# Optimization experiments

Hardware: AMD Instinct MI355X
Metric: run time of the kernel (lower is better)

The kernel has to match this reference:

```python
import jax, jax.numpy as jnp
import numpy as np

SEQ, B, T = 512, 1024, 48

def setup_inputs() -> dict:
    key = jax.random.key(0)
    k1, k2, k3, k4, k5 = jax.random.split(key, 5)
    return {
        "emissions": jax.random.normal(k1, (SEQ, B, T), dtype=jnp.float32),
        "tags": jax.random.randint(k2, (SEQ, B), 0, T, dtype=jnp.int64),
        "mask": jnp.ones((SEQ, B), dtype=jnp.int32),
        "start_transitions": jax.random.uniform(k3, (T,), minval=-0.1, maxval=0.1, dtype=jnp.float32),
        "end_transitions": jax.random.uniform(k4, (T,), minval=-0.1, maxval=0.1, dtype=jnp.float32),
        "transitions": jax.random.uniform(k5, (T, T), minval=-0.1, maxval=0.1, dtype=jnp.float32),
    }

def _score(emissions, tags, maskf, start_transitions, end_transitions, transitions):
    # numerator: score of the given tag path
    seq_len, batch = tags.shape
    emit = jnp.take_along_axis(emissions, tags[:, :, None], axis=2)[:, :, 0]  # (S,B)
    trans = transitions[tags[:-1], tags[1:]]  # (S-1,B)
    score = start_transitions[tags[0]] + emit[0]
    score = score + jnp.sum((trans + emit[1:]) * maskf[1:], axis=0)
    seq_ends = maskf.astype(jnp.int32).sum(axis=0) - 1  # (B,)
    last_tags = tags[seq_ends, jnp.arange(batch)]
    return score + end_transitions[last_tags]

def _normalizer(emissions, maskb, start_transitions, end_transitions, transitions):
    # forward algorithm: sequential logsumexp recurrence
    init = start_transitions + emissions[0]  # (B,T)

    def step(score, inp):
        emis_i, mask_i = inp  # (B,T), (B,)
        # score[b, prev] + transitions[prev, next] + emis_i[b, next]
        nxt = jax.nn.logsumexp(score[:, :, None] + transitions[None, :, :] + emis_i[:, None, :], axis=1)
        score = jnp.where(mask_i[:, None], nxt, score)
        return score, None

    score, _ = jax.lax.scan(step, init, (emissions[1:], maskb[1:]))
    return jax.nn.logsumexp(score + end_transitions, axis=1)

def reference(emissions, tags, mask, start_transitions, end_transitions, transitions):
    maskf = mask.astype(emissions.dtype)
    maskb = mask.astype(bool)
    num = _score(emissions, tags, maskf, start_transitions, end_transitions, transitions)
    den = _normalizer(emissions, maskb, start_transitions, end_transitions, transitions)
    llh = num - den  # (B,)
    return llh.mean()  # reduction='mean'
```

## Files before the change

### kernel.cpp

```cpp
#include <hip/hip_runtime.h>


constexpr int SEQ = 512, BN = 1024, TT = 48;
constexpr int CH = 8;
#define LOG2E 1.44269504088896340736f
#define LN2   0.69314718055994530942f

typedef int i32x4 __attribute__((ext_vector_type(4)));
typedef _Float16 h16x2 __attribute__((ext_vector_type(2)));

__device__ __forceinline__ float fexp2(float x) { return __builtin_amdgcn_exp2f(x); }
__device__ __forceinline__ float flog2(float x) { return __builtin_amdgcn_logf(x); }
__device__ __forceinline__ float rlane(float v, int i) {
    return __int_as_float(__builtin_amdgcn_readlane(__float_as_int(v), i));
}
__device__ __forceinline__ float dppswap(float v) {
    return __int_as_float(__builtin_amdgcn_mov_dpp(__float_as_int(v), 0xB1, 0xF, 0xF, true));
}
__device__ __forceinline__ float fdot2(int a, int b, float c) {
#if __has_builtin(__builtin_amdgcn_fdot2)
    return __builtin_amdgcn_fdot2(__builtin_bit_cast(h16x2, a),
                                  __builtin_bit_cast(h16x2, b), c, false);
#else
    float r;
    asm("v_dot2_f32_f16 %0, %1, %2, %3" : "=v"(r) : "v"(a), "v"(b), "v"(c));
    return r;
#endif
}

__global__ __launch_bounds__(128, 4) void crf_fwd(
    const float* __restrict__ emis, const int* __restrict__ tags,
    const int* __restrict__ mask, const float* __restrict__ start_t,
    const float* __restrict__ end_t, const float* __restrict__ trans,
    float* __restrict__ ws)
{
    __shared__ __align__(16) float smem[1600];

    const int tid  = threadIdx.x;
    const int wid  = tid >> 6;
    const int lane = tid & 63;
    const int cid  = blockIdx.x * 2 + wid;
    const int b    = cid & 1023;
    const int seg  = cid >> 10;
    const int cstart = seg ? (16 * seg - 1) : 0;
    const int cend   = 16 * (seg + 1);
    const int wbase  = wid * 768;
    int* pb = (int*)(smem + 1536) + wid * 32;

    const bool jv = (lane < TT);
    const int jc = jv ? lane : (TT - 1);
    const int l7 = lane & 7;

    _Float16* lh = (_Float16*)smem;
    for (int i = tid; i < TT * TT; i += 128) lh[i] = (_Float16)trans[i];
    __syncthreads();
    int Epk[24];
#pragma unroll
    for (int k = 0; k < 24; ++k) {
        const float a  = fexp2((float)lh[(2 * k) * TT + jc] * LOG2E);
        const float bb = fexp2((float)lh[(2 * k + 1) * TT + jc] * LOG2E);
        _Float16 h0 = (_Float16)a, h1 = (_Float16)bb;
        Epk[k] = (int)((unsigned)__builtin_bit_cast(unsigned short, h0) |
                       ((unsigned)__builtin_bit_cast(unsigned short, h1) << 16));
    }
#pragma unroll
    for (int k = 0; k < 24; ++k)
        asm volatile("" : "+v"(Epk[k]));
    const float st = start_t[jc];
    const float en = end_t[jc];
    __syncthreads();

    int offs[2];
#pragma unroll
    for (int k = 0; k < 2; ++k) {
        const int g = k * 64 + lane;
        const int r = g / 12, j4 = g % 12;
        offs[k] = r * (BN * TT * 4) + j4 * 16;
    }

#define STAGE_CHUNK(cc, buf)                                                   \
    {                                                                          \
        const char* cb = (const char*)emis + ((size_t)(cc) * CH * BN + b) * (TT * 4); \
        __builtin_amdgcn_global_load_lds(                                      \
            (const __attribute__((address_space(1))) void*)(cb + offs[0]),     \
            (__attribute__((address_space(3))) void*)(&smem[wbase + (buf) * 384]), \
            16, 0, 0);                                                         \
        if (lane < 32)                                                         \
            __builtin_amdgcn_global_load_lds(                                  \
                (const __attribute__((address_space(1))) void*)(cb + offs[1]), \
                (__attribute__((address_space(3))) void*)(&smem[wbase + (buf) * 384 + 256]), \
                16, 0, 0);                                                     \
    }

    STAGE_CHUNK(cstart, 0);
    int tgv = tags[(size_t)(cstart * CH + l7) * BN + b];
    int mkv = mask[(size_t)(cstart * CH + l7) * BN + b];

    asm volatile("s_waitcnt vmcnt(0)" ::: "memory");
    __builtin_amdgcn_sched_barrier(0);

    float r, numpart;
    int la, carry_tag;
    if (seg == 0) {
        const int tag0 = tags[b];
        const float e00 = smem[wbase + jc];
        r = jv ? fexp2(fmaf(st + e00, LOG2E, -6.0f)) : 0.0f;
        la = 6;
        numpart = (lane == tag0) ? (st + e00) : 0.f;
        carry_tag = tag0;
    } else {
        r = jv ? 1.0f : 0.0f;
        la = 0;
        numpart = 0.f;
        carry_tag = 0;
    }
    float numtr = 0.f, numem = 0.f, W = 0.f;
    int mcount = 0;

    STAGE_CHUNK(cstart + 1, 1);
    int tgn = tags[(size_t)((cstart + 1) * CH + l7) * BN + b];
    int mkn = mask[(size_t)((cstart + 1) * CH + l7) * BN + b];

    int cur = 0;

#pragma unroll 1
    for (int c = cstart; c < cend; ++c) {
#pragma unroll
        for (int k = 0; k < 24; ++k)
            asm volatile("" : "+v"(Epk[k]));

        const int tbase = c * CH;
        const float* ebc = smem + wbase + cur * 384;
        const bool warm = (c < 16 * seg);

        const int tmv = (lane < 8 && mkv && (tbase + lane) > 0) ? tgv : -1;
        const unsigned long long vmword = __ballot(tmv >= 0);
        int tprev = __shfl_up(tgv, 1, 64);
        if (lane == 0) tprev = carry_tag;
        if (!warm) {
            if (tmv >= 0) {
                numtr += trans[tprev * TT + tgv];
                numem += ebc[lane * TT + tgv];
            }
            mcount += __popcll(__ballot(lane < 8 && mkv));
        }
        carry_tag = __builtin_amdgcn_readlane(tgv, 7);
        la += 6 * (int)__popcll(vmword);

        const unsigned gm = (unsigned)vmword & 0xFFu;
        {
            const float r0 = rlane(r, 0);
            const int m = ((__float_as_int(r0) >> 23) & 0xFF) - 127;
            const float scl = __int_as_float((127 - m) << 23);
            r *= scl;
            la += m;
        }

        float emul[8];
#pragma unroll
        for (int u = 0; u < 8; ++u)
            emul[u] = fexp2(fmaf(ebc[u * TT + jc], LOG2E, -6.0f));

#pragma unroll
        for (int u = 0; u < 8; ++u) {
            const float rx = dppswap(r);
            const int pkw = __builtin_bit_cast(int,
                __builtin_amdgcn_cvt_pkrtz(r, rx));
            if (jv && !(lane & 1)) pb[lane >> 1] = pkw;
            asm volatile("" ::: "memory");
            const i32x4* pv = (const i32x4*)pb;
            float q0 = 0.f, q1 = 0.f, q2 = 0.f, q3 = 0.f;
#pragma unroll
            for (int k = 0; k < 6; ++k) {
                const i32x4 w = pv[k];
                q0 = fdot2(w.x, Epk[4 * k],     q0);
                q1 = fdot2(w.y, Epk[4 * k + 1], q1);
                q2 = fdot2(w.z, Epk[4 * k + 2], q2);
                q3 = fdot2(w.w, Epk[4 * k + 3], q3);
            }
            const float q = (q0 + q1) + (q2 + q3);
            const bool commit = (gm >> u) & 1u;
            r = commit ? (q * emul[u]) : r;
        }

        asm volatile("s_waitcnt vmcnt(0)" ::: "memory");
        __builtin_amdgcn_sched_barrier(0);
        cur ^= 1;
        tgv = tgn; mkv = mkn;
        if (c + 2 < cend) {
            STAGE_CHUNK(c + 2, cur ^ 1);
            tgn = tags[(size_t)((c + 2) * CH + l7) * BN + b];
            mkn = mask[(size_t)((c + 2) * CH + l7) * BN + b];
        }
        if (seg && c == 16 * seg - 1) {
            float sv = jv ? r : 0.f, se = sv;
#pragma unroll
            for (int d = 1; d < 64; d <<= 1)
                se += __shfl_xor(se, d, 64);
            W = (flog2(se) + (float)la) * LN2;
        }
    }

    float num = numpart + numtr + numem;
#pragma unroll
    for (int d = 1; d < 64; d <<= 1)
        num += __shfl_xor(num, d, 64);

    float sv = jv ? r : 0.f;
    if (seg == 3) sv = jv ? (r * fexp2(en * LOG2E)) : 0.f;
    float se = sv;
#pragma unroll
    for (int d = 1; d < 64; d <<= 1)
        se += __shfl_xor(se, d, 64);
    const float B = (flog2(se) + (float)la) * LN2;

    if (lane == 0) {
        ws[seg * 1024 + b]           = num;
        ws[4096 + seg * 1024 + b]    = B;
        ws[8192 + seg * 1024 + b]    = W;
        ws[12288 + seg * 1024 + b]   = (float)mcount;
    }
#undef STAGE_CHUNK
}

__global__ __launch_bounds__(256) void reduce_mean(
    const float* __restrict__ ws, const int* __restrict__ tags,
    const float* __restrict__ end_t, float* __restrict__ out)
{
    const int tid = threadIdx.x;
    float v = 0.f;
#pragma unroll
    for (int k = 0; k < 4; ++k) {
        const int b = tid + 256 * k;
        float num = 0.f, den = 0.f, mcf = 0.f;
#pragma unroll
        for (int s = 0; s < 4; ++s) {
            num += ws[s * 1024 + b];
            den += ws[4096 + s * 1024 + b] - ws[8192 + s * 1024 + b];
            mcf += ws[12288 + s * 1024 + b];
        }
        const int mc = (int)mcf;
        const int lt = tags[(size_t)(mc - 1) * BN + b];
        v += num + end_t[lt] - den;
    }
#pragma unroll
    for (int d = 1; d < 64; d <<= 1)
        v += __shfl_xor(v, d, 64);
    __shared__ float acc[4];
    if ((tid & 63) == 0) acc[tid >> 6] = v;
    __syncthreads();
    if (tid == 0) out[0] = (acc[0] + acc[1] + acc[2] + acc[3]) * (1.f / 1024.f);
}

extern "C" void kernel_launch(void* const* d_in, const int* in_sizes, int n_in,
                              void* d_out, int out_size, void* d_ws, size_t ws_size,
                              hipStream_t stream)
{
    const float* emis    = (const float*)d_in[0];
    const int*   tags    = (const int*)d_in[1];
    const int*   mask    = (const int*)d_in[2];
    const float* start_t = (const float*)d_in[3];
    const float* end_t   = (const float*)d_in[4];
    const float* trans   = (const float*)d_in[5];
    float* ws  = (float*)d_ws;
    float* out = (float*)d_out;

    crf_fwd<<<dim3(2048), dim3(128), 0, stream>>>(emis, tags, mask, start_t, end_t, trans, ws);
    reduce_mean<<<dim3(1), dim3(256), 0, stream>>>(ws, tags, end_t, out);
}
```

Baseline: 63.44 us.

## Process two batch rows per wavefront to interleave independent recurrences

Each wavefront now runs the forward recurrence for two batch elements at once, sharing the register-resident exp(transitions) matrix and interleaving two independent dependency chains, which gives more instruction-level parallelism. The grid is halved to 1024 blocks and LDS per block is doubled to hold both emission staging buffers and packed score buffers. The aim is to hide the latency of the serial LDS-write/read/dot chain per step. The cost is fewer wavefronts for latency hiding, higher register pressure and more LDS per block, which may lower occupancy.

```diff
diff --git a/kernel.cpp b/kernel.cpp
--- a/kernel.cpp
+++ b/kernel.cpp
@@ -34,18 +34,21 @@
     const float* __restrict__ end_t, const float* __restrict__ trans,
     float* __restrict__ ws)
 {
-    __shared__ __align__(16) float smem[1600];
+    __shared__ __align__(16) float smem[3200];
 
     const int tid  = threadIdx.x;
     const int wid  = tid >> 6;
     const int lane = tid & 63;
     const int cid  = blockIdx.x * 2 + wid;
-    const int b    = cid & 1023;
-    const int seg  = cid >> 10;
+    const int seg  = cid >> 9;
+    const int bp   = cid & 511;
+    const int bA   = bp * 2, bB = bp * 2 + 1;
     const int cstart = seg ? (16 * seg - 1) : 0;
     const int cend   = 16 * (seg + 1);
-    const int wbase  = wid * 768;
-    int* pb = (int*)(smem + 1536) + wid * 32;
+    const int wbA = wid * 1536;
+    const int wbB = wid * 1536 + 768;
+    int* pbA = (int*)(smem + 3072) + wid * 64;
+    int* pbB = pbA + 32;
 
     const bool jv = (lane < TT);
     const int jc = jv ? lane : (TT - 1);
@@ -78,48 +81,58 @@
         offs[k] = r * (BN * TT * 4) + j4 * 16;
     }
 
-#define STAGE_CHUNK(cc, buf)                                                   \
+#define STAGE_CHUNK(cc, bb_, base, buf)                                        \
     {                                                                          \
-        const char* cb = (const char*)emis + ((size_t)(cc) * CH * BN + b) * (TT * 4); \
+        const char* cb = (const char*)emis + ((size_t)(cc) * CH * BN + (bb_)) * (TT * 4); \
         __builtin_amdgcn_global_load_lds(                                      \
             (const __attribute__((address_space(1))) void*)(cb + offs[0]),     \
-            (__attribute__((address_space(3))) void*)(&smem[wbase + (buf) * 384]), \
+            (__attribute__((address_space(3))) void*)(&smem[(base) + (buf) * 384]), \
             16, 0, 0);                                                         \
         if (lane < 32)                                                         \
             __builtin_amdgcn_global_load_lds(                                  \
                 (const __attribute__((address_space(1))) void*)(cb + offs[1]), \
-                (__attribute__((address_space(3))) void*)(&smem[wbase + (buf) * 384 + 256]), \
+                (__attribute__((address_space(3))) void*)(&smem[(base) + (buf) * 384 + 256]), \
                 16, 0, 0);                                                     \
     }
 
-    STAGE_CHUNK(cstart, 0);
-    int tgv = tags[(size_t)(cstart * CH + l7) * BN + b];
-    int mkv = mask[(size_t)(cstart * CH + l7) * BN + b];
+    STAGE_CHUNK(cstart, bA, wbA, 0);
+    STAGE_CHUNK(cstart, bB, wbB, 0);
+    int tgvA = tags[(size_t)(cstart * CH + l7) * BN + bA];
+    int mkvA = mask[(size_t)(cstart * CH + l7) * BN + bA];
+    int tgvB = tags[(size_t)(cstart * CH + l7) * BN + bB];
+    int mkvB = mask[(size_t)(cstart * CH + l7) * BN + bB];
 
     asm volatile("s_waitcnt vmcnt(0)" ::: "memory");
     __builtin_amdgcn_sched_barrier(0);
 
-    float r, numpart;
-    int la, carry_tag;
+    float rA, rB, numpartA, numpartB;
+    int laA, laB, ctagA, ctagB;
     if (seg == 0) {
-        const int tag0 = tags[b];
-        const float e00 = smem[wbase + jc];
-        r = jv ? fexp2(fmaf(st + e00, LOG2E, -6.0f)) : 0.0f;
-        la = 6;
-        numpart = (lane == tag0) ? (st + e00) : 0.f;
-        carry_tag = tag0;
+        const int t0A = tags[bA], t0B = tags[bB];
+        const float eA = smem[wbA + jc], eB = smem[wbB + jc];
+        rA = jv ? fexp2(fmaf(st + eA, LOG2E, -6.0f)) : 0.0f;
+        rB = jv ? fexp2(fmaf(st + eB, LOG2E, -6.0f)) : 0.0f;
+        laA = laB = 6;
+        numpartA = (lane == t0A) ? (st + eA) : 0.f;
+        numpartB = (lane == t0B) ? (st + eB) : 0.f;
+        ctagA = t0A; ctagB = t0B;
     } else {
-        r = jv ? 1.0f : 0.0f;
-        la = 0;
-        numpart = 0.f;
-        carry_tag = 0;
-    }
-    float numtr = 0.f, numem = 0.f, W = 0.f;
-    int mcount = 0;
-
-    STAGE_CHUNK(cstart + 1, 1);
-    int tgn = tags[(size_t)((cstart + 1) * CH + l7) * BN + b];
-    int mkn = mask[(size_t)((cstart + 1) * CH + l7) * BN + b];
+        rA = jv ? 1.0f : 0.0f;
+        rB = jv ? 1.0f : 0.0f;
+        laA = laB = 0;
+        numpartA = numpartB = 0.f;
+        ctagA = ctagB = 0;
+    }
+    float numtrA = 0.f, numemA = 0.f, WA = 0.f;
+    float numtrB = 0.f, numemB = 0.f, WB = 0.f;
+    int mcA = 0, mcB = 0;
+
+    STAGE_CHUNK(cstart + 1, bA, wbA, 1);
+    STAGE_CHUNK(cstart + 1, bB, wbB, 1);
+    int tgnA = tags[(size_t)((cstart + 1) * CH + l7) * BN + bA];
+    int mknA = mask[(size_t)((cstart + 1) * CH + l7) * BN + bA];
+    int tgnB = tags[(size_t)((cstart + 1) * CH + l7) * BN + bB];
+    int mknB = mask[(size_t)((cstart + 1) * CH + l7) * BN + bB];
 
     int cur = 0;
 
@@ -130,95 +143,147 @@
             asm volatile("" : "+v"(Epk[k]));
 
         const int tbase = c * CH;
-        const float* ebc = smem + wbase + cur * 384;
+        const float* ebA = smem + wbA + cur * 384;
+        const float* ebB = smem + wbB + cur * 384;
         const bool warm = (c < 16 * seg);
 
-        const int tmv = (lane < 8 && mkv && (tbase + lane) > 0) ? tgv : -1;
-        const unsigned long long vmword = __ballot(tmv >= 0);
-        int tprev = __shfl_up(tgv, 1, 64);
-        if (lane == 0) tprev = carry_tag;
+        const int tmvA = (lane < 8 && mkvA && (tbase + lane) > 0) ? tgvA : -1;
+        const int tmvB = (lane < 8 && mkvB && (tbase + lane) > 0) ? tgvB : -1;
+        const unsigned long long vwA = __ballot(tmvA >= 0);
+        const unsigned long long vwB = __ballot(tmvB >= 0);
+        int tpA = __shfl_up(tgvA, 1, 64);
+        int tpB = __shfl_up(tgvB, 1, 64);
+        if (lane == 0) { tpA = ctagA; tpB = ctagB; }
         if (!warm) {
-            if (tmv >= 0) {
-                numtr += trans[tprev * TT + tgv];
-                numem += ebc[lane * TT + tgv];
-            }
-            mcount += __popcll(__ballot(lane < 8 && mkv));
-        }
-        carry_tag = __builtin_amdgcn_readlane(tgv, 7);
-        la += 6 * (int)__popcll(vmword);
-
-        const unsigned gm = (unsigned)vmword & 0xFFu;
+            if (tmvA >= 0) {
+                numtrA += trans[tpA * TT + tgvA];
+                numemA += ebA[lane * TT + tgvA];
+            }
+            if (tmvB >= 0) {
+                numtrB += trans[tpB * TT + tgvB];
+                numemB += ebB[lane * TT + tgvB];
+            }
+            mcA += __popcll(__ballot(lane < 8 && mkvA));
+            mcB += __popcll(__ballot(lane < 8 && mkvB));
+        }
+        ctagA = __builtin_amdgcn_readlane(tgvA, 7);
+        ctagB = __builtin_amdgcn_readlane(tgvB, 7);
+        laA += 6 * (int)__popcll(vwA);
+        laB += 6 * (int)__popcll(vwB);
+
+        const unsigned gmA = (unsigned)vwA & 0xFFu;
+        const unsigned gmB = (unsigned)vwB & 0xFFu;
         {
-            const float r0 = rlane(r, 0);
-            const int m = ((__float_as_int(r0) >> 23) & 0xFF) - 127;
-            const float scl = __int_as_float((127 - m) << 23);
-            r *= scl;
-            la += m;
-        }
-
-        float emul[8];
-#pragma unroll
-        for (int u = 0; u < 8; ++u)
-            emul[u] = fexp2(fmaf(ebc[u * TT + jc], LOG2E, -6.0f));
-
+            const float r0A = rlane(rA, 0);
+            const int mA = ((__float_as_int(r0A) >> 23) & 0xFF) - 127;
+            rA *= __int_as_float((127 - mA) << 23);
+            laA += mA;
+            const float r0B = rlane(rB, 0);
+            const int mB = ((__float_as_int(r0B) >> 23) & 0xFF) - 127;
+            rB *= __int_as_float((127 - mB) << 23);
+            laB += mB;
+        }
+
+        float emA[8], emB[8];
 #pragma unroll
         for (int u = 0; u < 8; ++u) {
-            const float rx = dppswap(r);
-            const int pkw = __builtin_bit_cast(int,
-                __builtin_amdgcn_cvt_pkrtz(r, rx));
-            if (jv && !(lane & 1)) pb[lane >> 1] = pkw;
+            emA[u] = fexp2(fmaf(ebA[u * TT + jc], LOG2E, -6.0f));
+            emB[u] = fexp2(fmaf(ebB[u * TT + jc], LOG2E, -6.0f));
+        }
+
+#pragma unroll
+        for (int u = 0; u < 8; ++u) {
+            const float rxA = dppswap(rA);
+            const int pkA = __builtin_bit_cast(int,
+                __builtin_amdgcn_cvt_pkrtz(rA, rxA));
+            const float rxB = dppswap(rB);
+            const int pkB = __builtin_bit_cast(int,
+                __builtin_amdgcn_cvt_pkrtz(rB, rxB));
+            if (jv && !(lane & 1)) {
+                pbA[lane >> 1] = pkA;
+                pbB[lane >> 1] = pkB;
+            }
             asm volatile("" ::: "memory");
-            const i32x4* pv = (const i32x4*)pb;
-            float q0 = 0.f, q1 = 0.f, q2 = 0.f, q3 = 0.f;
+            const i32x4* pvA = (const i32x4*)pbA;
+            const i32x4* pvB = (const i32x4*)pbB;
+            float a0 = 0.f, a1 = 0.f, a2 = 0.f, a3 = 0.f;
+            float b0 = 0.f, b1 = 0.f, b2 = 0.f, b3 = 0.f;
 #pragma unroll
             for (int k = 0; k < 6; ++k) {
-                const i32x4 w = pv[k];
-                q0 = fdot2(w.x, Epk[4 * k],     q0);
-                q1 = fdot2(w.y, Epk[4 * k + 1], q1);
-                q2 = fdot2(w.z, Epk[4 * k + 2], q2);
-                q3 = fdot2(w.w, Epk[4 * k + 3], q3);
-            }
-            const float q = (q0 + q1) + (q2 + q3);
-            const bool commit = (gm >> u) & 1u;
-            r = commit ? (q * emul[u]) : r;
+                const i32x4 wA = pvA[k];
+                a0 = fdot2(wA.x, Epk[4 * k],     a0);
+                a1 = fdot2(wA.y, Epk[4 * k + 1], a1);
+                a2 = fdot2(wA.z, Epk[4 * k + 2], a2);
+                a3 = fdot2(wA.w, Epk[4 * k + 3], a3);
+            }
+#pragma unroll
+            for (int k = 0; k < 6; ++k) {
+                const i32x4 wB = pvB[k];
+                b0 = fdot2(wB.x, Epk[4 * k],     b0);
+                b1 = fdot2(wB.y, Epk[4 * k + 1], b1);
+                b2 = fdot2(wB.z, Epk[4 * k + 2], b2);
+                b3 = fdot2(wB.w, Epk[4 * k + 3], b3);
+            }
+            const float qA = (a0 + a1) + (a2 + a3);
+            const float qB = (b0 + b1) + (b2 + b3);
+            rA = ((gmA >> u) & 1u) ? (qA * emA[u]) : rA;
+            rB = ((gmB >> u) & 1u) ? (qB * emB[u]) : rB;
         }
 
         asm volatile("s_waitcnt vmcnt(0)" ::: "memory");
         __builtin_amdgcn_sched_barrier(0);
         cur ^= 1;
-        tgv = tgn; mkv = mkn;
+        tgvA = tgnA; mkvA = mknA; tgvB = tgnB; mkvB = mknB;
         if (c + 2 < cend) {
-            STAGE_CHUNK(c + 2, cur ^ 1);
-            tgn = tags[(size_t)((c + 2) * CH + l7) * BN + b];
-            mkn = mask[(size_t)((c + 2) * CH + l7) * BN + b];
+            STAGE_CHUNK(c + 2, bA, wbA, cur ^ 1);
+            STAGE_CHUNK(c + 2, bB, wbB, cur ^ 1);
+            tgnA = tags[(size_t)((c + 2) * CH + l7) * BN + bA];
+            mknA = mask[(size_t)((c + 2) * CH + l7) * BN + bA];
+            tgnB = tags[(size_t)((c + 2) * CH + l7) * BN + bB];
+            mknB = mask[(size_t)((c + 2) * CH + l7) * BN + bB];
         }
         if (seg && c == 16 * seg - 1) {
-            float sv = jv ? r : 0.f, se = sv;
-#pragma unroll
-            for (int d = 1; d < 64; d <<= 1)
-                se += __shfl_xor(se, d, 64);
-            W = (flog2(se) + (float)la) * LN2;
-        }
-    }
-
-    float num = numpart + numtr + numem;
-#pragma unroll
-    for (int d = 1; d < 64; d <<= 1)
-        num += __shfl_xor(num, d, 64);
-
-    float sv = jv ? r : 0.f;
-    if (seg == 3) sv = jv ? (r * fexp2(en * LOG2E)) : 0.f;
-    float se = sv;
-#pragma unroll
-    for (int d = 1; d < 64; d <<= 1)
-        se += __shfl_xor(se, d, 64);
-    const float B = (flog2(se) + (float)la) * LN2;
+            float svA = jv ? rA : 0.f, seA = svA;
+            float svB = jv ? rB : 0.f, seB = svB;
+#pragma unroll
+            for (int d = 1; d < 64; d <<= 1) {
+                seA += __shfl_xor(seA, d, 64);
+                seB += __shfl_xor(seB, d, 64);
+            }
+            WA = (flog2(seA) + (float)laA) * LN2;
+            WB = (flog2(seB) + (float)laB) * LN2;
+        }
+    }
+
+    float numA = numpartA + numtrA + numemA;
+    float numB = numpartB + numtrB + numemB;
+    float svA = jv ? rA : 0.f;
+    float svB = jv ? rB : 0.f;
+    if (seg == 3) {
+        const float ee = fexp2(en * LOG2E);
+        svA = jv ? (rA * ee) : 0.f;
+        svB = jv ? (rB * ee) : 0.f;
+    }
+    float seA = svA, seB = svB;
+#pragma unroll
+    for (int d = 1; d < 64; d <<= 1) {
+        numA += __shfl_xor(numA, d, 64);
+        numB += __shfl_xor(numB, d, 64);
+        seA  += __shfl_xor(seA, d, 64);
+        seB  += __shfl_xor(seB, d, 64);
+    }
+    const float BA = (flog2(seA) + (float)laA) * LN2;
+    const float BB = (flog2(seB) + (float)laB) * LN2;
 
     if (lane == 0) {
-        ws[seg * 1024 + b]           = num;
-        ws[4096 + seg * 1024 + b]    = B;
-        ws[8192 + seg * 1024 + b]    = W;
-        ws[12288 + seg * 1024 + b]   = (float)mcount;
+        ws[seg * 1024 + bA]          = numA;
+        ws[4096 + seg * 1024 + bA]   = BA;
+        ws[8192 + seg * 1024 + bA]   = WA;
+        ws[12288 + seg * 1024 + bA]  = (float)mcA;
+        ws[seg * 1024 + bB]          = numB;
+        ws[4096 + seg * 1024 + bB]   = BB;
+        ws[8192 + seg * 1024 + bB]   = WB;
+        ws[12288 + seg * 1024 + bB]  = (float)mcB;
     }
 #undef STAGE_CHUNK
 }
@@ -265,6 +330,6 @@
     float* ws  = (float*)d_ws;
     float* out = (float*)d_out;
 
-    crf_fwd<<<dim3(2048), dim3(128), 0, stream>>>(emis, tags, mask, start_t, end_t, trans, ws);
+    crf_fwd<<<dim3(1024), dim3(128), 0, stream>>>(emis, tags, mask, start_t, end_t, trans, ws);
     reduce_mean<<<dim3(1), dim3(256), 0, stream>>>(ws, tags, end_t, out);
 }
```

After: 75.61 us. +19.2%, slower.
